# Optimization experiments

Measured on AMD Instinct MI355X. Metric: run time of the kernel, lower is better.

## Reference

```python
import jax, jax.numpy as jnp
import numpy as np

DIM, HEADS, WH, WW, MLAT, MLON = 512, 8, 8, 8, 32, 64
N = WH * WW
B = MLAT * MLON
PER_LAT = (2 * WH - 1) * (2 * WW - 1)  # 225


def _make_rel_idx():
    # Swin 2D relative position index inside one window
    ch, cw = np.arange(WH), np.arange(WW)
    coords = np.stack(np.meshgrid(ch, cw, indexing='ij')).reshape(2, -1)  # (2, N)
    rel = coords[:, :, None] - coords[:, None, :]                          # (2, N, N)
    rel = rel.transpose(1, 2, 0).astype(np.int64)
    rel[..., 0] += WH - 1
    rel[..., 1] += WW - 1
    rel[..., 0] *= 2 * WW - 1
    idx2d = rel.sum(-1)                                                    # (N, N)
    # earth-specific: each lat row i gets its own 225-entry slab; lon diff is 0
    idx = idx2d[None] + np.arange(MLAT)[:, None, None] * PER_LAT           # (Mlat, N, N)
    idx = np.broadcast_to(idx[:, None], (MLAT, MLON, N, N)).reshape(B, N, N)
    return jnp.asarray(idx.astype(np.int32))


def setup_inputs() -> dict:
    key = jax.random.key(0)
    k = jax.random.split(key, 5)
    x = jax.random.normal(k[0], (B, N, DIM), dtype=jnp.float32)
    w_qkv = jax.random.normal(k[1], (3 * DIM, DIM), dtype=jnp.float32) * 0.02
    b_qkv = jnp.zeros((3 * DIM,), dtype=jnp.float32)
    w_proj = jax.random.normal(k[2], (DIM, DIM), dtype=jnp.float32) * 0.02
    b_proj = jnp.zeros((DIM,), dtype=jnp.float32)
    bias_table = jax.random.normal(k[3], (MLAT * PER_LAT, HEADS), dtype=jnp.float32) * 0.02
    return {
        'x': x, 'w_qkv': w_qkv, 'b_qkv': b_qkv,
        'w_proj': w_proj, 'b_proj': b_proj,
        'bias_table': bias_table, 'rel_idx': _make_rel_idx(),
    }


def reference(x, w_qkv, b_qkv, w_proj, b_proj, bias_table, rel_idx):
    Bn, Nn, C = x.shape
    D = C // HEADS
    qkv = (x @ w_qkv.T + b_qkv).reshape(Bn, Nn, 3, HEADS, D)
    q = jnp.transpose(qkv[:, :, 0], (0, 2, 1, 3))  # (B, H, N, D)
    k = jnp.transpose(qkv[:, :, 1], (0, 2, 1, 3))
    v = jnp.transpose(qkv[:, :, 2], (0, 2, 1, 3))
    # gather learned earth bias: (B, N, N, H) -> (B, H, N, N)
    bias = jnp.transpose(bias_table[rel_idx], (0, 3, 1, 2))
    scale = D ** -0.5  # SDPA default scale (qk_scale is None)
    attn = jax.nn.softmax(jnp.einsum('bhnd,bhmd->bhnm', q, k) * scale + bias, axis=-1)
    out = jnp.einsum('bhnm,bhmd->bhnd', attn, v)
    out = jnp.transpose(out, (0, 2, 1, 3)).reshape(Bn, Nn, C)
    return out @ w_proj.T + b_proj
```

## Files before the change

kernel.cpp:

```cpp
#include <hip/hip_runtime.h>
#include <stdint.h>

typedef __attribute__((ext_vector_type(8))) short short8;
typedef __attribute__((ext_vector_type(4))) short short4v;
typedef __attribute__((ext_vector_type(4))) float float4v;

__device__ __forceinline__ short f2bf(float f) {
  uint32_t u = __builtin_bit_cast(uint32_t, f);
  u += 0x7FFFu + ((u >> 16) & 1u);
  return (short)(u >> 16);
}

#define XPITCH 520
#define QPITCH 72

__global__ void prep_weights(const float* __restrict__ wq, const float* __restrict__ wp,
                             short* __restrict__ wq_b, short* __restrict__ wp_b) {
  int i = blockIdx.x * blockDim.x + threadIdx.x;
  int stride = gridDim.x * blockDim.x;
  for (int j = i; j < 786432 / 4; j += stride) {
    float4 v = ((const float4*)wq)[j];
    short4v t = {f2bf(v.x), f2bf(v.y), f2bf(v.z), f2bf(v.w)};
    ((short4v*)wq_b)[j] = t;
  }
  for (int j = i; j < 262144 / 4; j += stride) {
    float4 v = ((const float4*)wp)[j];
    short4v t = {f2bf(v.x), f2bf(v.y), f2bf(v.z), f2bf(v.w)};
    ((short4v*)wp_b)[j] = t;
  }
}

__global__ __launch_bounds__(512, 2)
void qkv_attn(const float* __restrict__ x, const short* __restrict__ wq,
              const float* __restrict__ bqkv, const float* __restrict__ btab,
              short* __restrict__ attn) {
  __shared__ short Xs[64 * XPITCH];
  __shared__ short Qs[2][64 * QPITCH];
  __shared__ short Ks[2][64 * QPITCH];
  __shared__ short Vt[2][64 * QPITCH];

  const int b    = blockIdx.x;
  const int tid  = threadIdx.x;
  const int lane = tid & 63;
  const int w    = tid >> 6;
  const int l16  = lane & 15;
  const int quad = lane >> 4;
  const int lat  = b >> 6;

  const float* xw = x + (size_t)b * (64 * 512);
  for (int c = tid; c < 64 * 128; c += 512) {
    int n = c >> 7, kc = c & 127;
    float4 v = *(const float4*)(xw + n * 512 + kc * 4);
    short4v t = {f2bf(v.x), f2bf(v.y), f2bf(v.z), f2bf(v.w)};
    *(short4v*)&Xs[n * XPITCH + kc * 4] = t;
  }
  __syncthreads();

  for (int h0 = 0; h0 < 8; h0 += 2) {
    for (int s = w; s < 24; s += 8) {
      const int hsel  = s / 12;
      const int rem   = s % 12;
      const int mat   = rem >> 2;
      const int strip = rem & 3;
      const int h     = h0 + hsel;
      const short* Wbase = wq + (mat * 512 + h * 64 + strip * 16) * 512;

      float4v acc[4] = {};
      if (mat < 2) {
        const short* Arow = Wbase + l16 * 512 + quad * 8;
        for (int kk = 0; kk < 512; kk += 32) {
          short8 a = *(const short8*)(Arow + kk);
#pragma unroll
          for (int t = 0; t < 4; ++t) {
            short8 bf = *(const short8*)&Xs[(t * 16 + l16) * XPITCH + kk + quad * 8];
            acc[t] = __builtin_amdgcn_mfma_f32_16x16x32_bf16(a, bf, acc[t], 0, 0, 0);
          }
        }
        float bias[4];
#pragma unroll
        for (int i = 0; i < 4; ++i)
          bias[i] = bqkv[mat * 512 + h * 64 + strip * 16 + quad * 4 + i];
        short* dst = (mat == 0) ? &Qs[hsel][0] : &Ks[hsel][0];
        const float scale = (mat == 0) ? 0.125f : 1.0f;
#pragma unroll
        for (int t = 0; t < 4; ++t) {
          int n = t * 16 + l16;
          short4v pk;
#pragma unroll
          for (int i = 0; i < 4; ++i) pk[i] = f2bf((acc[t][i] + bias[i]) * scale);
          *(short4v*)&dst[n * QPITCH + strip * 16 + quad * 4] = pk;
        }
      } else {
        const short* Brow = Wbase + l16 * 512 + quad * 8;
        for (int kk = 0; kk < 512; kk += 32) {
          short8 bf = *(const short8*)(Brow + kk);
#pragma unroll
          for (int t = 0; t < 4; ++t) {
            short8 a = *(const short8*)&Xs[(t * 16 + l16) * XPITCH + kk + quad * 8];
            acc[t] = __builtin_amdgcn_mfma_f32_16x16x32_bf16(a, bf, acc[t], 0, 0, 0);
          }
        }
        float bias = bqkv[1024 + h * 64 + strip * 16 + l16];
#pragma unroll
        for (int t = 0; t < 4; ++t) {
          short4v pk;
#pragma unroll
          for (int i = 0; i < 4; ++i) pk[i] = f2bf(acc[t][i] + bias);
          *(short4v*)&Vt[hsel][(strip * 16 + l16) * QPITCH + t * 16 + quad * 4] = pk;
        }
      }
    }
    __syncthreads();

    {
      const int hsel = w >> 2;
      const int h    = h0 + hsel;
      const int n0   = (w & 3) * 16;

      float4v s4[4] = {};
#pragma unroll
      for (int kd = 0; kd < 64; kd += 32) {
        short8 a = *(const short8*)&Qs[hsel][(n0 + l16) * QPITCH + kd + quad * 8];
#pragma unroll
        for (int t = 0; t < 4; ++t) {
          short8 bf = *(const short8*)&Ks[hsel][(t * 16 + l16) * QPITCH + kd + quad * 8];
          s4[t] = __builtin_amdgcn_mfma_f32_16x16x32_bf16(a, bf, s4[t], 0, 0, 0);
        }
      }
#pragma unroll
      for (int t = 0; t < 4; ++t) {
        int m = t * 16 + l16;
#pragma unroll
        for (int i = 0; i < 4; ++i) {
          int n = n0 + quad * 4 + i;
          int idx = ((n >> 3) - (m >> 3) + 7) * 15 + ((n & 7) - (m & 7) + 7) + lat * 225;
          s4[t][i] += btab[idx * 8 + h];
        }
      }
      float p[4][4];
#pragma unroll
      for (int i = 0; i < 4; ++i) {
        float mx = fmaxf(fmaxf(s4[0][i], s4[1][i]), fmaxf(s4[2][i], s4[3][i]));
        mx = fmaxf(mx, __shfl_xor(mx, 1));
        mx = fmaxf(mx, __shfl_xor(mx, 2));
        mx = fmaxf(mx, __shfl_xor(mx, 4));
        mx = fmaxf(mx, __shfl_xor(mx, 8));
        float e0 = __expf(s4[0][i] - mx), e1 = __expf(s4[1][i] - mx);
        float e2 = __expf(s4[2][i] - mx), e3 = __expf(s4[3][i] - mx);
        float sm = e0 + e1 + e2 + e3;
        sm += __shfl_xor(sm, 1);
        sm += __shfl_xor(sm, 2);
        sm += __shfl_xor(sm, 4);
        sm += __shfl_xor(sm, 8);
        float inv = 1.0f / sm;
        p[0][i] = e0 * inv; p[1][i] = e1 * inv; p[2][i] = e2 * inv; p[3][i] = e3 * inv;
      }
#pragma unroll
      for (int t = 0; t < 4; ++t)
#pragma unroll
        for (int i = 0; i < 4; ++i)
          Qs[hsel][(n0 + quad * 4 + i) * QPITCH + t * 16 + l16] = f2bf(p[t][i]);
      __syncthreads();

      float4v o4[4] = {};
#pragma unroll
      for (int km = 0; km < 64; km += 32) {
        short8 a = *(const short8*)&Qs[hsel][(n0 + l16) * QPITCH + km + quad * 8];
#pragma unroll
        for (int t = 0; t < 4; ++t) {
          short8 bf = *(const short8*)&Vt[hsel][(t * 16 + l16) * QPITCH + km + quad * 8];
          o4[t] = __builtin_amdgcn_mfma_f32_16x16x32_bf16(a, bf, o4[t], 0, 0, 0);
        }
      }
      short* ob = attn + (size_t)b * (64 * 512);
#pragma unroll
      for (int t = 0; t < 4; ++t)
#pragma unroll
        for (int i = 0; i < 4; ++i)
          ob[(n0 + quad * 4 + i) * 512 + h * 64 + t * 16 + l16] = f2bf(o4[t][i]);
    }
    __syncthreads();
  }
}

__global__ __launch_bounds__(256, 3)
void proj_gemm(const short* __restrict__ attn, const short* __restrict__ wp,
               const float* __restrict__ bproj, float* __restrict__ out) {
  __shared__ short As[128 * 32];
  __shared__ short Bs[128 * 32];
  const int n0   = blockIdx.x * 128;
  const int m0   = blockIdx.y * 128;
  const int tid  = threadIdx.x;
  const int lane = tid & 63;
  const int w    = tid >> 6;
  const int l16  = lane & 15;
  const int quad = lane >> 4;
  const int wm   = w >> 1, wn = w & 1;

  float4v acc[4][4] = {};

  for (int kk = 0; kk < 512; kk += 32) {
#pragma unroll
    for (int r = 0; r < 2; ++r) {
      int c = tid + r * 256;
      int row = c >> 2, kc = c & 3;
      *(uint4*)&As[c * 8] = *(const uint4*)(attn + (size_t)(m0 + row) * 512 + kk + kc * 8);
      *(uint4*)&Bs[c * 8] = *(const uint4*)(wp + (size_t)(n0 + row) * 512 + kk + kc * 8);
    }
    __syncthreads();
    short8 a[4], bf[4];
#pragma unroll
    for (int ti = 0; ti < 4; ++ti)
      a[ti] = *(const short8*)&As[(wm * 64 + ti * 16 + l16) * 32 + quad * 8];
#pragma unroll
    for (int tj = 0; tj < 4; ++tj)
      bf[tj] = *(const short8*)&Bs[(wn * 64 + tj * 16 + l16) * 32 + quad * 8];
#pragma unroll
    for (int ti = 0; ti < 4; ++ti)
#pragma unroll
      for (int tj = 0; tj < 4; ++tj)
        acc[ti][tj] = __builtin_amdgcn_mfma_f32_16x16x32_bf16(a[ti], bf[tj], acc[ti][tj], 0, 0, 0);
    __syncthreads();
  }

  float bj[4];
#pragma unroll
  for (int tj = 0; tj < 4; ++tj) bj[tj] = bproj[n0 + wn * 64 + tj * 16 + l16];
#pragma unroll
  for (int ti = 0; ti < 4; ++ti)
#pragma unroll
    for (int i = 0; i < 4; ++i) {
      size_t rowoff = (size_t)(m0 + wm * 64 + ti * 16 + quad * 4 + i) * 512;
#pragma unroll
      for (int tj = 0; tj < 4; ++tj)
        out[rowoff + n0 + wn * 64 + tj * 16 + l16] = acc[ti][tj][i] + bj[tj];
    }
}

extern "C" void kernel_launch(void* const* d_in, const int* in_sizes, int n_in,
                              void* d_out, int out_size, void* d_ws, size_t ws_size,
                              hipStream_t stream) {
  const float* x     = (const float*)d_in[0];
  const float* wqkv  = (const float*)d_in[1];
  const float* bqkv  = (const float*)d_in[2];
  const float* wproj = (const float*)d_in[3];
  const float* bproj = (const float*)d_in[4];
  const float* btab  = (const float*)d_in[5];
  float* out = (float*)d_out;

  short* wq_b = (short*)d_ws;
  short* wp_b = wq_b + 786432;
  short* attn = wp_b + 262144;

  prep_weights<<<256, 256, 0, stream>>>(wqkv, wproj, wq_b, wp_b);
  qkv_attn<<<2048, 512, 0, stream>>>(x, wq_b, bqkv, btab, attn);
  proj_gemm<<<dim3(4, 1024), 256, 0, stream>>>(attn, wp_b, bproj, out);
}
```

Baseline: 1.036 ms.

## Fuse output projection into attention kernel and retile QKV GEMM per wave

Fuses the output projection into the per-window attention kernel. Each head's bf16 output is kept in registers, written into the reused X tile in shared memory, and multiplied by the projection weights in the same block, so the separate proj_gemm launch and the global attn buffer round trip go away. The QKV projection is retiled so waves 0-3 each compute a full 64x64 Q or K tile and waves 4-7 compute 64x32 V tiles. This cuts redundant weight loads but gives the Q/K waves twice the work of the V waves. It also drops the barrier between writing P and the PV product, relying on each wave reading only its own rows, and it adds register pressure from holding all head outputs.

After: 1.054 ms. No clear change (+1.7%).

```diff
diff --git a/kernel.cpp b/kernel.cpp
--- a/kernel.cpp
+++ b/kernel.cpp
@@ -10,6 +10,8 @@
   u += 0x7FFFu + ((u >> 16) & 1u);
   return (short)(u >> 16);
 }
+
+#define MFMA __builtin_amdgcn_mfma_f32_16x16x32_bf16
 
 #define XPITCH 520
 #define QPITCH 72
@@ -31,21 +33,24 @@
 }
 
 __global__ __launch_bounds__(512, 2)
-void qkv_attn(const float* __restrict__ x, const short* __restrict__ wq,
-              const float* __restrict__ bqkv, const float* __restrict__ btab,
-              short* __restrict__ attn) {
+void fused_attn(const float* __restrict__ x, const short* __restrict__ wq,
+                const short* __restrict__ wp, const float* __restrict__ bqkv,
+                const float* __restrict__ bproj, const float* __restrict__ btab,
+                float* __restrict__ out) {
   __shared__ short Xs[64 * XPITCH];
   __shared__ short Qs[2][64 * QPITCH];
   __shared__ short Ks[2][64 * QPITCH];
   __shared__ short Vt[2][64 * QPITCH];
 
-  const int b    = blockIdx.x;
-  const int tid  = threadIdx.x;
-  const int lane = tid & 63;
-  const int w    = tid >> 6;
-  const int l16  = lane & 15;
-  const int quad = lane >> 4;
-  const int lat  = b >> 6;
+  const int b     = blockIdx.x;
+  const int tid   = threadIdx.x;
+  const int lane  = tid & 63;
+  const int w     = tid >> 6;
+  const int l16   = lane & 15;
+  const int quad  = lane >> 4;
+  const int lat   = b >> 6;
+  const int hsel2 = w >> 2;
+  const int n0    = (w & 3) * 16;
 
   const float* xw = x + (size_t)b * (64 * 512);
   for (int c = tid; c < 64 * 128; c += 512) {
@@ -56,75 +61,92 @@
   }
   __syncthreads();
 
-  for (int h0 = 0; h0 < 8; h0 += 2) {
-    for (int s = w; s < 24; s += 8) {
-      const int hsel  = s / 12;
-      const int rem   = s % 12;
-      const int mat   = rem >> 2;
-      const int strip = rem & 3;
-      const int h     = h0 + hsel;
-      const short* Wbase = wq + (mat * 512 + h * 64 + strip * 16) * 512;
-
-      float4v acc[4] = {};
-      if (mat < 2) {
-        const short* Arow = Wbase + l16 * 512 + quad * 8;
-        for (int kk = 0; kk < 512; kk += 32) {
-          short8 a = *(const short8*)(Arow + kk);
-#pragma unroll
-          for (int t = 0; t < 4; ++t) {
-            short8 bf = *(const short8*)&Xs[(t * 16 + l16) * XPITCH + kk + quad * 8];
-            acc[t] = __builtin_amdgcn_mfma_f32_16x16x32_bf16(a, bf, acc[t], 0, 0, 0);
-          }
-        }
+  short4v Opk[4][4];
+
+#pragma unroll
+  for (int r = 0; r < 4; ++r) {
+    const int h0 = 2 * r;
+    if (w < 4) {
+      const int mat = w >> 1;
+      const int hs  = w & 1;
+      const int h   = h0 + hs;
+      const short* Wb = wq + (size_t)(mat * 512 + h * 64) * 512;
+      float4v acc[4][4] = {};
+      for (int kk = 0; kk < 512; kk += 32) {
+        short8 a[4], bb[4];
+#pragma unroll
+        for (int ti = 0; ti < 4; ++ti)
+          a[ti] = *(const short8*)(Wb + (ti * 16 + l16) * 512 + kk + quad * 8);
+#pragma unroll
+        for (int tj = 0; tj < 4; ++tj)
+          bb[tj] = *(const short8*)&Xs[(tj * 16 + l16) * XPITCH + kk + quad * 8];
+#pragma unroll
+        for (int ti = 0; ti < 4; ++ti)
+#pragma unroll
+          for (int tj = 0; tj < 4; ++tj)
+            acc[ti][tj] = MFMA(a[ti], bb[tj], acc[ti][tj], 0, 0, 0);
+      }
+      short* dst = (mat == 0) ? &Qs[hs][0] : &Ks[hs][0];
+      const float scale = (mat == 0) ? 0.125f : 1.0f;
+#pragma unroll
+      for (int ti = 0; ti < 4; ++ti) {
         float bias[4];
 #pragma unroll
         for (int i = 0; i < 4; ++i)
-          bias[i] = bqkv[mat * 512 + h * 64 + strip * 16 + quad * 4 + i];
-        short* dst = (mat == 0) ? &Qs[hsel][0] : &Ks[hsel][0];
-        const float scale = (mat == 0) ? 0.125f : 1.0f;
-#pragma unroll
-        for (int t = 0; t < 4; ++t) {
-          int n = t * 16 + l16;
+          bias[i] = bqkv[mat * 512 + h * 64 + ti * 16 + quad * 4 + i];
+#pragma unroll
+        for (int tj = 0; tj < 4; ++tj) {
           short4v pk;
 #pragma unroll
-          for (int i = 0; i < 4; ++i) pk[i] = f2bf((acc[t][i] + bias[i]) * scale);
-          *(short4v*)&dst[n * QPITCH + strip * 16 + quad * 4] = pk;
-        }
-      } else {
-        const short* Brow = Wbase + l16 * 512 + quad * 8;
-        for (int kk = 0; kk < 512; kk += 32) {
-          short8 bf = *(const short8*)(Brow + kk);
-#pragma unroll
-          for (int t = 0; t < 4; ++t) {
-            short8 a = *(const short8*)&Xs[(t * 16 + l16) * XPITCH + kk + quad * 8];
-            acc[t] = __builtin_amdgcn_mfma_f32_16x16x32_bf16(a, bf, acc[t], 0, 0, 0);
-          }
-        }
-        float bias = bqkv[1024 + h * 64 + strip * 16 + l16];
-#pragma unroll
-        for (int t = 0; t < 4; ++t) {
+          for (int i = 0; i < 4; ++i) pk[i] = f2bf((acc[ti][tj][i] + bias[i]) * scale);
+          *(short4v*)&dst[(tj * 16 + l16) * QPITCH + ti * 16 + quad * 4] = pk;
+        }
+      }
+    } else {
+      const int hs = (w >> 1) & 1;
+      const int h  = h0 + hs;
+      const int d0 = (w & 1) * 32;
+      const short* Wb = wq + (size_t)(1024 + h * 64 + d0) * 512;
+      float4v acc[4][2] = {};
+      for (int kk = 0; kk < 512; kk += 32) {
+        short8 a[4], bb[2];
+#pragma unroll
+        for (int ti = 0; ti < 4; ++ti)
+          a[ti] = *(const short8*)&Xs[(ti * 16 + l16) * XPITCH + kk + quad * 8];
+#pragma unroll
+        for (int tj = 0; tj < 2; ++tj)
+          bb[tj] = *(const short8*)(Wb + (tj * 16 + l16) * 512 + kk + quad * 8);
+#pragma unroll
+        for (int ti = 0; ti < 4; ++ti)
+#pragma unroll
+          for (int tj = 0; tj < 2; ++tj)
+            acc[ti][tj] = MFMA(a[ti], bb[tj], acc[ti][tj], 0, 0, 0);
+      }
+#pragma unroll
+      for (int tj = 0; tj < 2; ++tj) {
+        float bias = bqkv[1024 + h * 64 + d0 + tj * 16 + l16];
+#pragma unroll
+        for (int ti = 0; ti < 4; ++ti) {
           short4v pk;
 #pragma unroll
-          for (int i = 0; i < 4; ++i) pk[i] = f2bf(acc[t][i] + bias);
-          *(short4v*)&Vt[hsel][(strip * 16 + l16) * QPITCH + t * 16 + quad * 4] = pk;
+          for (int i = 0; i < 4; ++i) pk[i] = f2bf(acc[ti][tj][i] + bias);
+          *(short4v*)&Vt[hs][(d0 + tj * 16 + l16) * QPITCH + ti * 16 + quad * 4] = pk;
         }
       }
     }
     __syncthreads();
 
     {
-      const int hsel = w >> 2;
-      const int h    = h0 + hsel;
-      const int n0   = (w & 3) * 16;
+      const int h = h0 + hsel2;
 
       float4v s4[4] = {};
 #pragma unroll
       for (int kd = 0; kd < 64; kd += 32) {
-        short8 a = *(const short8*)&Qs[hsel][(n0 + l16) * QPITCH + kd + quad * 8];
+        short8 a = *(const short8*)&Qs[hsel2][(n0 + l16) * QPITCH + kd + quad * 8];
 #pragma unroll
         for (int t = 0; t < 4; ++t) {
-          short8 bf = *(const short8*)&Ks[hsel][(t * 16 + l16) * QPITCH + kd + quad * 8];
-          s4[t] = __builtin_amdgcn_mfma_f32_16x16x32_bf16(a, bf, s4[t], 0, 0, 0);
+          short8 bf = *(const short8*)&Ks[hsel2][(t * 16 + l16) * QPITCH + kd + quad * 8];
+          s4[t] = MFMA(a, bf, s4[t], 0, 0, 0);
         }
       }
 #pragma unroll
@@ -159,82 +181,71 @@
       for (int t = 0; t < 4; ++t)
 #pragma unroll
         for (int i = 0; i < 4; ++i)
-          Qs[hsel][(n0 + quad * 4 + i) * QPITCH + t * 16 + l16] = f2bf(p[t][i]);
-      __syncthreads();
+          Qs[hsel2][(n0 + quad * 4 + i) * QPITCH + t * 16 + l16] = f2bf(p[t][i]);
 
       float4v o4[4] = {};
 #pragma unroll
       for (int km = 0; km < 64; km += 32) {
-        short8 a = *(const short8*)&Qs[hsel][(n0 + l16) * QPITCH + km + quad * 8];
+        short8 a = *(const short8*)&Qs[hsel2][(n0 + l16) * QPITCH + km + quad * 8];
 #pragma unroll
         for (int t = 0; t < 4; ++t) {
-          short8 bf = *(const short8*)&Vt[hsel][(t * 16 + l16) * QPITCH + km + quad * 8];
-          o4[t] = __builtin_amdgcn_mfma_f32_16x16x32_bf16(a, bf, o4[t], 0, 0, 0);
-        }
-      }
-      short* ob = attn + (size_t)b * (64 * 512);
-#pragma unroll
-      for (int t = 0; t < 4; ++t)
-#pragma unroll
-        for (int i = 0; i < 4; ++i)
-          ob[(n0 + quad * 4 + i) * 512 + h * 64 + t * 16 + l16] = f2bf(o4[t][i]);
+          short8 bf = *(const short8*)&Vt[hsel2][(t * 16 + l16) * QPITCH + km + quad * 8];
+          o4[t] = MFMA(a, bf, o4[t], 0, 0, 0);
+        }
+      }
+#pragma unroll
+      for (int t = 0; t < 4; ++t) {
+        short4v pk;
+#pragma unroll
+        for (int i = 0; i < 4; ++i) pk[i] = f2bf(o4[t][i]);
+        Opk[r][t] = pk;
+      }
     }
     __syncthreads();
   }
-}
-
-__global__ __launch_bounds__(256, 3)
-void proj_gemm(const short* __restrict__ attn, const short* __restrict__ wp,
-               const float* __restrict__ bproj, float* __restrict__ out) {
-  __shared__ short As[128 * 32];
-  __shared__ short Bs[128 * 32];
-  const int n0   = blockIdx.x * 128;
-  const int m0   = blockIdx.y * 128;
-  const int tid  = threadIdx.x;
-  const int lane = tid & 63;
-  const int w    = tid >> 6;
-  const int l16  = lane & 15;
-  const int quad = lane >> 4;
-  const int wm   = w >> 1, wn = w & 1;
-
-  float4v acc[4][4] = {};
-
-  for (int kk = 0; kk < 512; kk += 32) {
-#pragma unroll
-    for (int r = 0; r < 2; ++r) {
-      int c = tid + r * 256;
-      int row = c >> 2, kc = c & 3;
-      *(uint4*)&As[c * 8] = *(const uint4*)(attn + (size_t)(m0 + row) * 512 + kk + kc * 8);
-      *(uint4*)&Bs[c * 8] = *(const uint4*)(wp + (size_t)(n0 + row) * 512 + kk + kc * 8);
+
+#pragma unroll
+  for (int r = 0; r < 4; ++r) {
+    const int cb = (2 * r + hsel2) * 64;
+#pragma unroll
+    for (int t = 0; t < 4; ++t)
+#pragma unroll
+      for (int i = 0; i < 4; ++i)
+        Xs[(n0 + quad * 4 + i) * XPITCH + cb + t * 16 + l16] = Opk[r][t][i];
+  }
+  __syncthreads();
+
+  {
+    const short* Wp = wp + (size_t)(w * 64) * 512;
+    float4v acc[4][4] = {};
+    for (int kk = 0; kk < 512; kk += 32) {
+      short8 a[4], bb[4];
+#pragma unroll
+      for (int ti = 0; ti < 4; ++ti)
+        a[ti] = *(const short8*)&Xs[(ti * 16 + l16) * XPITCH + kk + quad * 8];
+#pragma unroll
+      for (int tj = 0; tj < 4; ++tj)
+        bb[tj] = *(const short8*)(Wp + (tj * 16 + l16) * 512 + kk + quad * 8);
+#pragma unroll
+      for (int ti = 0; ti < 4; ++ti)
+#pragma unroll
+        for (int tj = 0; tj < 4; ++tj)
+          acc[ti][tj] = MFMA(a[ti], bb[tj], acc[ti][tj], 0, 0, 0);
     }
-    __syncthreads();
-    short8 a[4], bf[4];
+    float bj[4];
+#pragma unroll
+    for (int tj = 0; tj < 4; ++tj) bj[tj] = bproj[w * 64 + tj * 16 + l16];
+    float* ob = out + (size_t)b * (64 * 512);
 #pragma unroll
     for (int ti = 0; ti < 4; ++ti)
-      a[ti] = *(const short8*)&As[(wm * 64 + ti * 16 + l16) * 32 + quad * 8];
-#pragma unroll
-    for (int tj = 0; tj < 4; ++tj)
-      bf[tj] = *(const short8*)&Bs[(wn * 64 + tj * 16 + l16) * 32 + quad * 8];
-#pragma unroll
-    for (int ti = 0; ti < 4; ++ti)
-#pragma unroll
-      for (int tj = 0; tj < 4; ++tj)
-        acc[ti][tj] = __builtin_amdgcn_mfma_f32_16x16x32_bf16(a[ti], bf[tj], acc[ti][tj], 0, 0, 0);
-    __syncthreads();
-  }
-
-  float bj[4];
-#pragma unroll
-  for (int tj = 0; tj < 4; ++tj) bj[tj] = bproj[n0 + wn * 64 + tj * 16 + l16];
-#pragma unroll
-  for (int ti = 0; ti < 4; ++ti)
-#pragma unroll
-    for (int i = 0; i < 4; ++i) {
-      size_t rowoff = (size_t)(m0 + wm * 64 + ti * 16 + quad * 4 + i) * 512;
-#pragma unroll
-      for (int tj = 0; tj < 4; ++tj)
-        out[rowoff + n0 + wn * 64 + tj * 16 + l16] = acc[ti][tj][i] + bj[tj];
-    }
+#pragma unroll
+      for (int i = 0; i < 4; ++i) {
+        const int row = (ti * 16 + quad * 4 + i) * 512;
+#pragma unroll
+        for (int tj = 0; tj < 4; ++tj)
+          ob[row + w * 64 + tj * 16 + l16] = acc[ti][tj][i] + bj[tj];
+      }
+  }
 }
 
 extern "C" void kernel_launch(void* const* d_in, const int* in_sizes, int n_in,
@@ -250,9 +261,7 @@
 
   short* wq_b = (short*)d_ws;
   short* wp_b = wq_b + 786432;
-  short* attn = wp_b + 262144;
 
   prep_weights<<<256, 256, 0, stream>>>(wqkv, wproj, wq_b, wp_b);
-  qkv_attn<<<2048, 512, 0, stream>>>(x, wq_b, bqkv, btab, attn);
-  proj_gemm<<<dim3(4, 1024), 256, 0, stream>>>(attn, wp_b, bproj, out);
-}
+  fused_attn<<<2048, 512, 0, stream>>>(x, wq_b, wp_b, bqkv, bproj, btab, out);
+}
```
